# Optimization experiments

Measured on AMD Instinct MI355X. Metric: run time of the kernel, lower is better.

## Reference

```python
import jax, jax.numpy as jnp
import numpy as np

NB_CLUSTERS = 128   # C: number of clusters (equal-size, sorted ids)
PTS_PER_CLUSTER = 1024  # P: points per cluster
DIM = 3


def setup_inputs() -> dict:
    key = jax.random.key(0)
    k1, k2 = jax.random.split(key)
    n = NB_CLUSTERS * PTS_PER_CLUSTER
    input_points = jax.random.normal(k1, (n, DIM), dtype=jnp.float32)
    output_points = jax.random.normal(k2, (n, DIM), dtype=jnp.float32)
    clusters = jnp.repeat(jnp.arange(NB_CLUSTERS, dtype=jnp.int32), PTS_PER_CLUSTER)
    return {
        "input_points": input_points,
        "input_clusters": clusters,
        "output_points": output_points,
        "output_clusters": clusters,
    }


def reference(input_points, input_clusters, output_points, output_clusters):
    # Original: nb_clusters = max(input_clusters); loop for i in range(nb_clusters)
    # -> the HIGHEST cluster id is excluded from the loss. Reproduced via mask.
    nb = jnp.max(input_clusters)  # == NB_CLUSTERS - 1
    a = input_points.reshape(NB_CLUSTERS, PTS_PER_CLUSTER, DIM)   # [C,P,3]
    b = output_points.reshape(NB_CLUSTERS, PTS_PER_CLUSTER, DIM)  # [C,P,3]

    # Pairwise squared distances per cluster: d[c,i,j] = ||a[c,i]-b[c,j]||^2
    d = (jnp.sum(a * a, axis=-1)[:, :, None]
         + jnp.sum(b * b, axis=-1)[:, None, :]
         - 2.0 * jnp.einsum('cid,cjd->cij', a, b))  # [C,P,P]

    # Indices computed under no_grad in the original (ints: no grad anyway).
    idx1 = jnp.argmin(d, axis=2)  # for each input point: nearest output point
    idx2 = jnp.argmin(d, axis=1)  # for each output point: nearest input point

    near_b = jnp.take_along_axis(b, idx1[..., None], axis=1)  # [C,P,3]
    near_a = jnp.take_along_axis(a, idx2[..., None], axis=1)  # [C,P,3]

    l1 = jnp.sum((a - near_b) ** 2, axis=(1, 2))  # [C]
    l2 = jnp.sum((b - near_a) ** 2, axis=(1, 2))  # [C]

    mask = (jnp.arange(NB_CLUSTERS) < nb).astype(a.dtype)  # exclude last cluster
    return jnp.sum(mask * (l1 + l2))
```

## Files before the change

kernel.cpp:

```cpp
#include <hip/hip_runtime.h>


#define PTS 1024
#define ACTIVE_CLUSTERS 127
#define QG   128
#define Q    8
#define SEG  8
#define TPB  1024
#define TSEG (PTS / SEG)

__global__ __launch_bounds__(TPB) void chamfer_kernel(
    const float* __restrict__ pts_in,
    const float* __restrict__ pts_out,
    float* __restrict__ out)
{
    const int c   = blockIdx.x >> 1;
    const int dir = blockIdx.x & 1;

    const float* __restrict__ query  = dir ? pts_out : pts_in;
    const float* __restrict__ target = dir ? pts_in  : pts_out;

    __shared__ __align__(16) float4 st[PTS];
    __shared__ float pm[SEG * Q * QG];

    const int tid = threadIdx.x;
    const int qi  = tid & (QG - 1);
    const int seg = tid >> 7;
    const size_t base = (size_t)c * PTS * 3;

    {
        const float* tp = target + base + (size_t)tid * 3;
        float x = tp[0], y = tp[1], z = tp[2];
        st[tid] = make_float4(x, y, z, fmaf(x, x, fmaf(y, y, z * z)));
    }

    float qx[Q], qy[Q], qz[Q], qn[Q], mn[Q];
    #pragma unroll
    for (int k = 0; k < Q; ++k) {
        const float* qp = query + base + (size_t)(k * QG + qi) * 3;
        float ax = qp[0], ay = qp[1], az = qp[2];
        qn[k] = fmaf(ax, ax, fmaf(ay, ay, az * az));
        qx[k] = -2.0f * ax;
        qy[k] = -2.0f * ay;
        qz[k] = -2.0f * az;
        mn[k] = 3.4e38f;
    }
    __syncthreads();

    const int j0 = seg * TSEG;
    #pragma unroll 4
    for (int jj = 0; jj < TSEG; jj += 2) {
        const float4 b0 = st[j0 + jj];
        const float4 b1 = st[j0 + jj + 1];
        #pragma unroll
        for (int k = 0; k < Q; ++k) {
            float s0 = fmaf(qx[k], b0.x, b0.w);
            s0 = fmaf(qy[k], b0.y, s0);
            s0 = fmaf(qz[k], b0.z, s0);
            float s1 = fmaf(qx[k], b1.x, b1.w);
            s1 = fmaf(qy[k], b1.y, s1);
            s1 = fmaf(qz[k], b1.z, s1);
            mn[k] = fminf(fminf(s0, s1), mn[k]);
        }
    }

    #pragma unroll
    for (int k = 0; k < Q; ++k)
        pm[(seg * Q + k) * QG + qi] = mn[k] + qn[k];
    __syncthreads();

    const int k2  = tid >> 7;
    const int qi2 = tid & (QG - 1);
    float v = 3.4e38f;
    #pragma unroll
    for (int s = 0; s < SEG; ++s)
        v = fminf(v, pm[(s * Q + k2) * QG + qi2]);

    #pragma unroll
    for (int off = 32; off > 0; off >>= 1)
        v += __shfl_down(v, off, 64);

    __shared__ float wsum[16];
    const int wave = tid >> 6;
    const int lane = tid & 63;
    if (lane == 0) wsum[wave] = v;
    __syncthreads();

    if (wave == 0) {
        float t = (lane < 16) ? wsum[lane] : 0.0f;
        #pragma unroll
        for (int off = 8; off > 0; off >>= 1)
            t += __shfl_down(t, off, 64);
        if (lane == 0) atomicAdd(out, t);
    }
}

extern "C" void kernel_launch(void* const* d_in, const int* in_sizes, int n_in,
                              void* d_out, int out_size, void* d_ws, size_t ws_size,
                              hipStream_t stream) {
    const float* input_points  = (const float*)d_in[0];
    const float* output_points = (const float*)d_in[2];
    float* out = (float*)d_out;

    hipMemsetAsync(out, 0, sizeof(float), stream);

    chamfer_kernel<<<dim3(ACTIVE_CLUSTERS * 2), dim3(TPB), 0, stream>>>(
        input_points, output_points, out);
}
```

Measured before the change: 83.36 us.

## Use packed FP32 FMAs, SoA shared layout, larger query tile, atomic min reduction

Target points now sit in separate x/y/z/norm shared arrays and are read four at a time, so distance terms for two targets are evaluated with packed two-wide FMAs. Each thread now owns 16 query points instead of 8 and scans one of 16 target segments. The per-segment partial-minimum array is replaced by shared atomicMin on the float bit pattern. The aim is to cut the ALU instruction count per point pair and the cost of the cross-segment reduction. This raises register pressure, and the unsigned atomicMin is only correct if the expanded distances stay non-negative, which rounding in the expansion may not guarantee.

```diff
diff --git a/kernel.cpp b/kernel.cpp
--- a/kernel.cpp
+++ b/kernel.cpp
@@ -1,13 +1,19 @@
 #include <hip/hip_runtime.h>
 
 
-#define PTS 1024
+#define PTS  1024
 #define ACTIVE_CLUSTERS 127
-#define QG   128
-#define Q    8
-#define SEG  8
+#define QG   64
+#define Q    16
+#define SEG  16
 #define TPB  1024
 #define TSEG (PTS / SEG)
+
+typedef float v2f __attribute__((ext_vector_type(2)));
+
+static __device__ __forceinline__ v2f splat2(float a) {
+    v2f r; r.x = a; r.y = a; return r;
+}
 
 __global__ __launch_bounds__(TPB) void chamfer_kernel(
     const float* __restrict__ pts_in,
@@ -20,18 +26,25 @@
     const float* __restrict__ query  = dir ? pts_out : pts_in;
     const float* __restrict__ target = dir ? pts_in  : pts_out;
 
-    __shared__ __align__(16) float4 st[PTS];
-    __shared__ float pm[SEG * Q * QG];
+    __shared__ __align__(16) float sx[PTS];
+    __shared__ __align__(16) float sy[PTS];
+    __shared__ __align__(16) float sz[PTS];
+    __shared__ __align__(16) float sh[PTS];
+    __shared__ unsigned colmin[PTS];
+    __shared__ float wsum[16];
 
     const int tid = threadIdx.x;
     const int qi  = tid & (QG - 1);
-    const int seg = tid >> 7;
+    const int seg = tid >> 6;
     const size_t base = (size_t)c * PTS * 3;
+
+    colmin[tid] = 0x7f7fffffu;
 
     {
         const float* tp = target + base + (size_t)tid * 3;
         float x = tp[0], y = tp[1], z = tp[2];
-        st[tid] = make_float4(x, y, z, fmaf(x, x, fmaf(y, y, z * z)));
+        sx[tid] = x; sy[tid] = y; sz[tid] = z;
+        sh[tid] = fmaf(x, x, fmaf(y, y, z * z));
     }
 
     float qx[Q], qy[Q], qz[Q], qn[Q], mn[Q];
@@ -48,39 +61,45 @@
     __syncthreads();
 
     const int j0 = seg * TSEG;
-    #pragma unroll 4
-    for (int jj = 0; jj < TSEG; jj += 2) {
-        const float4 b0 = st[j0 + jj];
-        const float4 b1 = st[j0 + jj + 1];
+    #pragma unroll 2
+    for (int jj = 0; jj < TSEG; jj += 4) {
+        const float4 bx = *(const float4*)&sx[j0 + jj];
+        const float4 by = *(const float4*)&sy[j0 + jj];
+        const float4 bz = *(const float4*)&sz[j0 + jj];
+        const float4 bh = *(const float4*)&sh[j0 + jj];
+        v2f bx01; bx01.x = bx.x; bx01.y = bx.y;
+        v2f bx23; bx23.x = bx.z; bx23.y = bx.w;
+        v2f by01; by01.x = by.x; by01.y = by.y;
+        v2f by23; by23.x = by.z; by23.y = by.w;
+        v2f bz01; bz01.x = bz.x; bz01.y = bz.y;
+        v2f bz23; bz23.x = bz.z; bz23.y = bz.w;
+        v2f bh01; bh01.x = bh.x; bh01.y = bh.y;
+        v2f bh23; bh23.x = bh.z; bh23.y = bh.w;
         #pragma unroll
         for (int k = 0; k < Q; ++k) {
-            float s0 = fmaf(qx[k], b0.x, b0.w);
-            s0 = fmaf(qy[k], b0.y, s0);
-            s0 = fmaf(qz[k], b0.z, s0);
-            float s1 = fmaf(qx[k], b1.x, b1.w);
-            s1 = fmaf(qy[k], b1.y, s1);
-            s1 = fmaf(qz[k], b1.z, s1);
-            mn[k] = fminf(fminf(s0, s1), mn[k]);
+            v2f s01 = __builtin_elementwise_fma(splat2(qx[k]), bx01, bh01);
+            s01 = __builtin_elementwise_fma(splat2(qy[k]), by01, s01);
+            s01 = __builtin_elementwise_fma(splat2(qz[k]), bz01, s01);
+            v2f s23 = __builtin_elementwise_fma(splat2(qx[k]), bx23, bh23);
+            s23 = __builtin_elementwise_fma(splat2(qy[k]), by23, s23);
+            s23 = __builtin_elementwise_fma(splat2(qz[k]), bz23, s23);
+            mn[k] = fminf(fminf(s01.x, s01.y), mn[k]);
+            mn[k] = fminf(fminf(s23.x, s23.y), mn[k]);
         }
     }
 
     #pragma unroll
-    for (int k = 0; k < Q; ++k)
-        pm[(seg * Q + k) * QG + qi] = mn[k] + qn[k];
+    for (int k = 0; k < Q; ++k) {
+        float v = mn[k] + qn[k];
+        atomicMin(&colmin[k * QG + qi], __float_as_uint(v));
+    }
     __syncthreads();
 
-    const int k2  = tid >> 7;
-    const int qi2 = tid & (QG - 1);
-    float v = 3.4e38f;
-    #pragma unroll
-    for (int s = 0; s < SEG; ++s)
-        v = fminf(v, pm[(s * Q + k2) * QG + qi2]);
-
+    float v = __uint_as_float(colmin[tid]);
     #pragma unroll
     for (int off = 32; off > 0; off >>= 1)
         v += __shfl_down(v, off, 64);
 
-    __shared__ float wsum[16];
     const int wave = tid >> 6;
     const int lane = tid & 63;
     if (lane == 0) wsum[wave] = v;
```

Result: slower. 143.6 us (+72.2%).
